# Optimization experiments

Measured on AMD Instinct MI355X. Metric: run time of the kernel, lower is better.

## Reference

```python
import jax, jax.numpy as jnp
import numpy as np
from jax import lax

NUM_GROUPS = 1024
GROUP_SIZE = 32
INIT_DIST = 1e10  # matches torch's 10000000000.0 init


def setup_inputs() -> dict:
    key = jax.random.key(0)
    k1, k2 = jax.random.split(key)
    x = jax.random.normal(k1, (1, 65536, 3), dtype=jnp.float32)
    features = jax.random.normal(k2, (1, 65536, 64), dtype=jnp.float32)
    return {"x": x, "features": features}


def _fps(xyz, npoint):
    # xyz: [B, N, 3] -> centers: [1, npoint, 3] (original code assumes B==1)
    B, N, _ = xyz.shape
    init_dist = jnp.full((B, N), INIT_DIST, dtype=xyz.dtype)
    init_far = jnp.zeros((B,), dtype=jnp.int32)  # deterministic start (torch uses randint)

    def step(carry, _):
        distance, farthest = carry
        centroid = jnp.take_along_axis(xyz, farthest[:, None, None], axis=1)  # [B,1,3]
        dist = jnp.sum((xyz - centroid) ** 2, axis=-1)  # [B,N]
        distance = jnp.minimum(distance, dist)
        new_far = jnp.argmax(distance, axis=-1).astype(jnp.int32)
        return (distance, new_far), farthest

    _, centroids = lax.scan(step, (init_dist, init_far), None, length=npoint)
    centroids = centroids.T  # [B, npoint]
    # original: fps_data = xyz[0, fps_idx].unsqueeze(0)  (B==1 assumption)
    return xyz[0, centroids[0]][None]  # [1, npoint, 3]


def _square_distance(src, dst):
    # src: [B,G,3], dst: [B,N,3] -> [B,G,N]
    d = -2.0 * jnp.einsum("bgc,bnc->bgn", src, dst)
    d += jnp.sum(src ** 2, -1)[:, :, None]
    d += jnp.sum(dst ** 2, -1)[:, None, :]
    return d


def reference(x, features):
    centers = _fps(x, NUM_GROUPS)                 # [1,G,3]
    distances = _square_distance(centers, x)      # [1,G,N]
    _, nb_idx = lax.top_k(-distances, GROUP_SIZE)  # smallest-k -> [1,G,M]
    F = features.shape[-1]
    flat_feat = features.reshape(-1, F)
    neighbors = flat_feat[nb_idx.reshape(-1)].reshape(1, -1, GROUP_SIZE, F)
    nearest_center_idx = jnp.argmin(distances, axis=1)  # [1,N]
    return neighbors, nearest_center_idx
```

## Files before the change

### kernel.cpp

```cpp
#include <hip/hip_runtime.h>
#include <stdint.h>

#define N_PTS   65536
#define N_GRP   1024
#define K_NB    32
#define F_DIM   64

#define FPS1_THR 1024
#define NCHUNK   1024
#define CPTS     64
#define NBINS    4096

#define F2_BLOCKS 16
#define F2_THR    512
#define F2_TT     (F2_BLOCKS*F2_THR)
#define F2_P      (N_PTS / F2_TT)

__device__ __forceinline__ unsigned long long packMinKey(float v, unsigned int idx) {
  unsigned int b = __float_as_uint(v);
  b = (b & 0x80000000u) ? ~b : (b | 0x80000000u);
  return ((unsigned long long)b << 32) | idx;
}
__device__ __forceinline__ float unpackMinVal(unsigned long long k) {
  unsigned int b = (unsigned int)(k >> 32);
  b = (b & 0x80000000u) ? (b & 0x7FFFFFFFu) : ~b;
  return __uint_as_float(b);
}
__device__ __forceinline__ unsigned spread4(unsigned b) {
  return (b & 1u) | ((b & 2u) << 2) | ((b & 4u) << 4) | ((b & 8u) << 6);
}
__device__ __forceinline__ unsigned morton_bid(float a, float b, float c) {
  const float S = 16.0f / 11.0f;
  int bx = (int)((a + 5.5f) * S);
  int by = (int)((b + 5.5f) * S);
  int bz = (int)((c + 5.5f) * S);
  bx = min(max(bx, 0), 15); by = min(max(by, 0), 15); bz = min(max(bz, 0), 15);
  return spread4((unsigned)bx) | (spread4((unsigned)by) << 1) | (spread4((unsigned)bz) << 2);
}

__global__ void __launch_bounds__(FPS1_THR)
fps_kernel(const float* __restrict__ x, float4* __restrict__ xs4,
           float* __restrict__ dd, float* __restrict__ centers)
{
  __shared__ __align__(16) char smem[40960];
  unsigned* sA = (unsigned*)smem;
  unsigned* sB = (unsigned*)(smem + 16384);
  unsigned long long* ckeys = (unsigned long long*)smem;
  unsigned* act = (unsigned*)(smem + 8192);
  float* bxl = (float*)(smem + 12288);
  float* bxh = bxl + 1024;
  float* byl = bxl + 2048;
  float* byh = bxl + 3072;
  float* bzl = bxl + 4096;
  float* bzh = bxl + 5120;
  __shared__ unsigned long long red[16];
  __shared__ int s_nact;

  const int tid = threadIdx.x, lane = tid & 63, wid = tid >> 6;

#pragma unroll
  for (int j = 0; j < NBINS/FPS1_THR; ++j) sA[tid + j*FPS1_THR] = 0u;
  __syncthreads();
  for (int i = tid; i < N_PTS; i += FPS1_THR) {
    float a = x[i*3+0], b = x[i*3+1], c = x[i*3+2];
    atomicAdd(&sA[morton_bid(a,b,c)], 1u);
  }
  __syncthreads();

  {
    unsigned* src = sA; unsigned* dst = sB;
    for (int off = 1; off < NBINS; off <<= 1) {
#pragma unroll
      for (int j = 0; j < NBINS/FPS1_THR; ++j) {
        int i = tid + j*FPS1_THR;
        unsigned v = src[i];
        if (i >= off) v += src[i-off];
        dst[i] = v;
      }
      __syncthreads();
      unsigned* t_ = src; src = dst; dst = t_;
    }
#pragma unroll
    for (int j = 0; j < NBINS/FPS1_THR; ++j) {
      int i = tid + j*FPS1_THR;
      sB[i] = (i == 0) ? 0u : sA[i-1];
    }
    __syncthreads();
  }

  for (int i = tid; i < N_PTS; i += FPS1_THR) {
    float a = x[i*3+0], b = x[i*3+1], c = x[i*3+2];
    unsigned pos = atomicAdd(&sB[morton_bid(a,b,c)], 1u);
    xs4[pos] = make_float4(a, b, c, __uint_as_float((unsigned)i));
    dd[pos]  = 1e10f;
  }
  __syncthreads();

  for (int cc = 0; cc < 64; ++cc) {
    const int c = wid*64 + cc;
    float4 f = xs4[c*CPTS + lane];
    float xl = f.x, xh = f.x, yl = f.y, yh = f.y, zl = f.z, zh = f.z;
#pragma unroll
    for (int off = 32; off; off >>= 1) {
      xl = fminf(xl, __shfl_xor(xl, off)); xh = fmaxf(xh, __shfl_xor(xh, off));
      yl = fminf(yl, __shfl_xor(yl, off)); yh = fmaxf(yh, __shfl_xor(yh, off));
      zl = fminf(zl, __shfl_xor(zl, off)); zh = fmaxf(zh, __shfl_xor(zh, off));
    }
    if (lane == 0) { bxl[c]=xl; bxh[c]=xh; byl[c]=yl; byh[c]=yh; bzl[c]=zl; bzh[c]=zh; }
  }
  __syncthreads();
  const float rxl = bxl[tid], rxh = bxh[tid];
  const float ryl = byl[tid], ryh = byh[tid];
  const float rzl = bzl[tid], rzh = bzh[tid];
  __syncthreads();

  if (tid == 0) s_nact = 0;
  __syncthreads();

  float cx = x[0], cy = x[1], cz = x[2];
  if (tid == 0) { centers[0] = cx; centers[1] = cy; centers[2] = cz; }
  float cdmax = 1e10f;

  for (int r = 1; r < N_GRP; ++r) {
    float dxl = fmaxf(fmaxf(rxl - cx, cx - rxh), 0.0f);
    float dyl = fmaxf(fmaxf(ryl - cy, cy - ryh), 0.0f);
    float dzl = fmaxf(fmaxf(rzl - cz, cz - rzh), 0.0f);
    float b2 = fmaf(dzl, dzl, fmaf(dyl, dyl, dxl*dxl));
    const bool active = b2 < cdmax * 1.0001f;
    const unsigned long long bal = __ballot(active);
    int base = 0;
    if (lane == 0) { int cnt = __popcll(bal); if (cnt) base = atomicAdd(&s_nact, cnt); }
    base = __shfl(base, 0);
    if (active) { int rank = __popcll(bal & ((1ull << lane) - 1ull)); act[base + rank] = (unsigned)tid; }
    __syncthreads();

    const int n = s_nact;
    const int sub = lane >> 4, li = lane & 15;
    for (int bj = wid*4; bj < n; bj += 64) {
      const int jdx = bj + sub;
      const int c = (jdx < n) ? (int)act[jdx] : -1;
      unsigned long long key = 0ull;
      if (c >= 0) {
        const int cb = c*CPTS;
#pragma unroll
        for (int t = 0; t < 4; ++t) {
          const int sidx = cb + li + 16*t;
          float4 f = xs4[sidx];
          float dk = dd[sidx];
          float e0 = f.x - cx, e1 = f.y - cy, e2 = f.z - cz;
          float dist = fmaf(e2,e2, fmaf(e1,e1, e0*e0));
          float dn = fminf(dk, dist);
          dd[sidx] = dn;
          unsigned long long kk = ((unsigned long long)__float_as_uint(dn) << 32)
                                | (unsigned long long)(0xFFFFFFFFu - __float_as_uint(f.w));
          if (kk > key) key = kk;
        }
      }
#pragma unroll
      for (int off = 1; off < 16; off <<= 1) {
        unsigned long long o = __shfl_xor(key, off);
        if (o > key) key = o;
      }
      if (c >= 0 && li == 0) ckeys[c] = key;
    }
    __syncthreads();

    unsigned long long kown = ckeys[tid];
    cdmax = __uint_as_float((unsigned)(kown >> 32));
    unsigned long long k = kown;
#pragma unroll
    for (int off = 32; off; off >>= 1) {
      unsigned long long o = __shfl_xor(k, off);
      if (o > k) k = o;
    }
    if (lane == 0) red[wid] = k;
    if (tid == 0) s_nact = 0;
    __syncthreads();
    unsigned long long k2 = red[lane & 15];
#pragma unroll
    for (int off = 1; off < 16; off <<= 1) {
      unsigned long long o = __shfl_xor(k2, off);
      if (o > k2) k2 = o;
    }
    const unsigned orig = 0xFFFFFFFFu - (unsigned)(k2 & 0xFFFFFFFFull);
    cx = x[orig*3+0]; cy = x[orig*3+1]; cz = x[orig*3+2];
    if (tid == 0) { centers[r*3+0]=cx; centers[r*3+1]=cy; centers[r*3+2]=cz; }
  }
}

__global__ void __launch_bounds__(F2_THR)
fps_safe_kernel(const float* __restrict__ x, unsigned long long* __restrict__ slots,
                unsigned int* __restrict__ cnts, float* __restrict__ centers)
{
  __shared__ unsigned long long red[F2_THR/64];
  const int t = blockIdx.x * F2_THR + threadIdx.x;
  float px[F2_P], py[F2_P], pz[F2_P], d[F2_P];
#pragma unroll
  for (int k = 0; k < F2_P; ++k) {
    int p = t + k * F2_TT;
    px[k] = x[p*3+0]; py[k] = x[p*3+1]; pz[k] = x[p*3+2];
    d[k] = 1e10f;
  }
  float cx = x[0], cy = x[1], cz = x[2];
  if (blockIdx.x == 0 && threadIdx.x == 0) {
    centers[0] = cx; centers[1] = cy; centers[2] = cz;
  }
  for (int r = 1; r < N_GRP; ++r) {
    unsigned long long best = 0ull;
#pragma unroll
    for (int k = 0; k < F2_P; ++k) {
      float e0 = px[k]-cx, e1 = py[k]-cy, e2 = pz[k]-cz;
      float dist = fmaf(e2,e2, fmaf(e1,e1, e0*e0));
      float dn = fminf(d[k], dist);
      d[k] = dn;
      unsigned long long pk = ((unsigned long long)__float_as_uint(dn) << 32)
                            | (0xFFFFFFFFu - (unsigned)(t + k*F2_TT));
      if (pk > best) best = pk;
    }
#pragma unroll
    for (int off = 32; off; off >>= 1) {
      unsigned long long o = __shfl_down(best, off);
      if (o > best) best = o;
    }
    const int wid = threadIdx.x >> 6;
    if ((threadIdx.x & 63) == 0) red[wid] = best;
    __syncthreads();
    if (threadIdx.x == 0) {
#pragma unroll
      for (int w = 1; w < F2_THR/64; ++w) if (red[w] > best) best = red[w];
      atomicMax(&slots[r], best);
      __hip_atomic_fetch_add(&cnts[r], 1u, __ATOMIC_RELEASE, __HIP_MEMORY_SCOPE_AGENT);
      while (__hip_atomic_load(&cnts[r], __ATOMIC_ACQUIRE, __HIP_MEMORY_SCOPE_AGENT) < F2_BLOCKS)
        __builtin_amdgcn_s_sleep(1);
      red[0] = __hip_atomic_load(&slots[r], __ATOMIC_RELAXED, __HIP_MEMORY_SCOPE_AGENT);
    }
    __syncthreads();
    const unsigned long long win = red[0];
    const int widx = (int)(0xFFFFFFFFu - (unsigned int)(win & 0xFFFFFFFFull));
    cx = x[widx*3+0]; cy = x[widx*3+1]; cz = x[widx*3+2];
    if (blockIdx.x == 0 && threadIdx.x == 0) {
      centers[r*3+0] = cx; centers[r*3+1] = cy; centers[r*3+2] = cz;
    }
    __syncthreads();
  }
}

#define TKT 256
#define CAP 3072

__global__ void __launch_bounds__(TKT)
topk_kernel(const float* __restrict__ x, const float* __restrict__ feat,
            const float* __restrict__ centers, float* __restrict__ out)
{
  __shared__ float cv[CAP];
  __shared__ int   ci[CAP];
  __shared__ int   s_cnt;
  __shared__ float s_thr;
  __shared__ float selv[K_NB];
  __shared__ int   seli[K_NB];

  const int g = blockIdx.x, tid = threadIdx.x;
  const float cx = centers[g*3+0], cy = centers[g*3+1], cz = centers[g*3+2];
  const float c2 = fmaf(cz,cz, fmaf(cy,cy, cx*cx));
  if (tid == 0) { s_cnt = 0; s_thr = __builtin_inff(); }
  __syncthreads();

  const int CH = N_PTS / (TKT*8);
  for (int chunk = 0; chunk < CH; ++chunk) {
    const float lthr = s_thr;
#pragma unroll
    for (int k = 0; k < 8; ++k) {
      int p = (chunk*8 + k)*TKT + tid;
      float q0 = x[p*3+0], q1 = x[p*3+1], q2 = x[p*3+2];
      float dot  = fmaf(cz,q2, fmaf(cy,q1, cx*q0));
      float pp   = fmaf(q2,q2, fmaf(q1,q1, q0*q0));
      float dist = fmaf(-2.0f, dot, c2) + pp;
      if (dist <= lthr) {
        int pos = atomicAdd(&s_cnt, 1);
        cv[pos] = dist; ci[pos] = p;
      }
    }
    __syncthreads();
    const int n = s_cnt;
    const bool last = (chunk == CH-1);
    if (n > (CAP - TKT*8) || last) {
      if (tid < 64) {
        for (int it = 0; it < K_NB; ++it) {
          unsigned long long lk = ~0ull;
          for (int j = tid; j < n; j += 64) {
            unsigned long long kk = packMinKey(cv[j], (unsigned)ci[j]);
            if (kk < lk) lk = kk;
          }
#pragma unroll
          for (int off = 32; off; off >>= 1) {
            unsigned long long o = __shfl_xor(lk, off);
            if (o < lk) lk = o;
          }
          const int mi = (int)(unsigned int)(lk & 0xFFFFFFFFull);
          for (int j = tid; j < n; j += 64)
            if (ci[j] == mi) cv[j] = __builtin_inff();
          if (tid == 0) { selv[it] = unpackMinVal(lk); seli[it] = mi; }
        }
      }
      __syncthreads();
      if (!last) {
        if (tid < K_NB) { cv[tid] = selv[tid]; ci[tid] = seli[tid]; }
        if (tid == 0)   { s_cnt = K_NB; s_thr = selv[K_NB-1]; }
        __syncthreads();
      }
    }
  }

  const long base = (long)g * (K_NB*F_DIM);
#pragma unroll
  for (int m = 0; m < (K_NB*F_DIM)/TKT; ++m) {
    int lin = m*TKT + tid;
    int j = lin >> 6, c = lin & 63;
    out[base + lin] = feat[(long)seli[j]*F_DIM + c];
  }
}

__global__ void __launch_bounds__(256)
argmin_kernel(const float* __restrict__ x, const float* __restrict__ centers,
              float* __restrict__ outIdx)
{
  __shared__ float scx[N_GRP], scy[N_GRP], scz[N_GRP], sc2[N_GRP];
  for (int i = threadIdx.x; i < N_GRP; i += 256) {
    float a = centers[i*3+0], b = centers[i*3+1], c = centers[i*3+2];
    scx[i]=a; scy[i]=b; scz[i]=c;
    sc2[i] = fmaf(c,c, fmaf(b,b, a*a));
  }
  __syncthreads();
  const int p = blockIdx.x*256 + threadIdx.x;
  const float q0 = x[p*3+0], q1 = x[p*3+1], q2 = x[p*3+2];
  const float pp = fmaf(q2,q2, fmaf(q1,q1, q0*q0));
  float best = __builtin_inff(); int bi = 0;
#pragma unroll 4
  for (int c = 0; c < N_GRP; ++c) {
    float dot  = fmaf(scz[c],q2, fmaf(scy[c],q1, scx[c]*q0));
    float dist = fmaf(-2.0f, dot, sc2[c]) + pp;
    if (dist < best) { best = dist; bi = c; }
  }
  outIdx[p] = (float)bi;
}

extern "C" void kernel_launch(void* const* d_in, const int* in_sizes, int n_in,
                              void* d_out, int out_size, void* d_ws, size_t ws_size,
                              hipStream_t stream)
{
  const float* x    = (const float*)d_in[0];
  const float* feat = (const float*)d_in[1];
  float* out = (float*)d_out;
  char* ws = (char*)d_ws;

  float* ctr = (float*)ws;
  const size_t DD_OFF  = 65536;
  const size_t XS_OFF  = DD_OFF + (size_t)N_PTS*4;
  const size_t NEED    = XS_OFF + (size_t)N_PTS*16;

  if (ws_size >= NEED) {
    float*  dd  = (float*)(ws + DD_OFF);
    float4* xs4 = (float4*)(ws + XS_OFF);
    hipLaunchKernelGGL(fps_kernel, dim3(1), dim3(FPS1_THR), 0, stream, x, xs4, dd, ctr);
  } else {
    unsigned long long* slots = (unsigned long long*)(ws + 16384);
    unsigned int*       cnts  = (unsigned int*)(ws + 24576);
    hipMemsetAsync(ws + 16384, 0, 12288, stream);
    hipLaunchKernelGGL(fps_safe_kernel, dim3(F2_BLOCKS), dim3(F2_THR), 0, stream,
                       x, slots, cnts, ctr);
  }
  hipLaunchKernelGGL(topk_kernel, dim3(N_GRP), dim3(TKT), 0, stream, x, feat, ctr, out);
  hipLaunchKernelGGL(argmin_kernel, dim3(N_PTS/256), dim3(256), 0, stream,
                     x, ctr, out + (size_t)N_GRP*K_NB*F_DIM);
}
```

Before: 2.986 ms.

## Replace shared active-list compaction with per-wave ballot loops and double-max keys

Each FPS iteration no longer builds a shared-memory list of active chunks with atomics. Each wave now processes its own interleaved chunks straight from its ballot mask, which drops one block-wide barrier and the s_nact atomic per iteration. The 64-bit argmax keys are packed as doubles so fmax replaces the compare-and-select on 64-bit integers. The risks are that work can be uneven across waves, since each wave only handles its own chunks, and that the key keeps only 16 bits of the original index, which relies on N being exactly 65536.

```diff
diff --git a/kernel.cpp b/kernel.cpp
--- a/kernel.cpp
+++ b/kernel.cpp
@@ -37,26 +37,32 @@
   bx = min(max(bx, 0), 15); by = min(max(by, 0), 15); bz = min(max(bz, 0), 15);
   return spread4((unsigned)bx) | (spread4((unsigned)by) << 1) | (spread4((unsigned)bz) << 2);
 }
+__device__ __forceinline__ double packKeyD(float d, unsigned orig, int c) {
+  unsigned long long k = ((unsigned long long)__float_as_uint(d) << 32)
+                       | ((unsigned long long)(0xFFFFu - (orig & 0xFFFFu)) << 16)
+                       | (unsigned long long)(unsigned)c;
+  return __longlong_as_double((long long)k);
+}
 
 __global__ void __launch_bounds__(FPS1_THR)
 fps_kernel(const float* __restrict__ x, float4* __restrict__ xs4,
            float* __restrict__ dd, float* __restrict__ centers)
 {
-  __shared__ __align__(16) char smem[40960];
-  unsigned* sA = (unsigned*)smem;
-  unsigned* sB = (unsigned*)(smem + 16384);
-  unsigned long long* ckeys = (unsigned long long*)smem;
-  unsigned* act = (unsigned*)(smem + 8192);
-  float* bxl = (float*)(smem + 12288);
+  __shared__ __align__(16) char smem[65536];
+  double* ckeys = (double*)smem;
+  float* bxl = (float*)(smem + 8192);
   float* bxh = bxl + 1024;
   float* byl = bxl + 2048;
   float* byh = bxl + 3072;
   float* bzl = bxl + 4096;
   float* bzh = bxl + 5120;
-  __shared__ unsigned long long red[16];
-  __shared__ int s_nact;
+  unsigned* sA = (unsigned*)(smem + 32768);
+  unsigned* sB = (unsigned*)(smem + 49152);
+  __shared__ double redd[16];
 
   const int tid = threadIdx.x, lane = tid & 63, wid = tid >> 6;
+  const int sub = lane >> 4, li = lane & 15;
+  const int cown = 16*lane + wid;
 
 #pragma unroll
   for (int j = 0; j < NBINS/FPS1_THR; ++j) sA[tid + j*FPS1_THR] = 0u;
@@ -109,13 +115,9 @@
     if (lane == 0) { bxl[c]=xl; bxh[c]=xh; byl[c]=yl; byh[c]=yh; bzl[c]=zl; bzh[c]=zh; }
   }
   __syncthreads();
-  const float rxl = bxl[tid], rxh = bxh[tid];
-  const float ryl = byl[tid], ryh = byh[tid];
-  const float rzl = bzl[tid], rzh = bzh[tid];
-  __syncthreads();
-
-  if (tid == 0) s_nact = 0;
-  __syncthreads();
+  const float rxl = bxl[cown], rxh = bxh[cown];
+  const float ryl = byl[cown], ryh = byh[cown];
+  const float rzl = bzl[cown], rzh = bzh[cown];
 
   float cx = x[0], cy = x[1], cz = x[2];
   if (tid == 0) { centers[0] = cx; centers[1] = cy; centers[2] = cz; }
@@ -127,19 +129,17 @@
     float dzl = fmaxf(fmaxf(rzl - cz, cz - rzh), 0.0f);
     float b2 = fmaf(dzl, dzl, fmaf(dyl, dyl, dxl*dxl));
     const bool active = b2 < cdmax * 1.0001f;
-    const unsigned long long bal = __ballot(active);
-    int base = 0;
-    if (lane == 0) { int cnt = __popcll(bal); if (cnt) base = atomicAdd(&s_nact, cnt); }
-    base = __shfl(base, 0);
-    if (active) { int rank = __popcll(bal & ((1ull << lane) - 1ull)); act[base + rank] = (unsigned)tid; }
-    __syncthreads();
-
-    const int n = s_nact;
-    const int sub = lane >> 4, li = lane & 15;
-    for (int bj = wid*4; bj < n; bj += 64) {
-      const int jdx = bj + sub;
-      const int c = (jdx < n) ? (int)act[jdx] : -1;
-      unsigned long long key = 0ull;
+    unsigned long long m = __ballot(active);
+
+    while (m) {
+      int b0 = __ffsll(m) - 1; m &= m - 1;
+      int b1 = -1, b2i = -1, b3 = -1;
+      if (m) { b1  = __ffsll(m) - 1; m &= m - 1; }
+      if (m) { b2i = __ffsll(m) - 1; m &= m - 1; }
+      if (m) { b3  = __ffsll(m) - 1; m &= m - 1; }
+      const int bb = (sub == 0) ? b0 : (sub == 1) ? b1 : (sub == 2) ? b2i : b3;
+      const int c = (bb >= 0) ? (16*bb + wid) : -1;
+      double key = 0.0;
       if (c >= 0) {
         const int cb = c*CPTS;
 #pragma unroll
@@ -151,38 +151,28 @@
           float dist = fmaf(e2,e2, fmaf(e1,e1, e0*e0));
           float dn = fminf(dk, dist);
           dd[sidx] = dn;
-          unsigned long long kk = ((unsigned long long)__float_as_uint(dn) << 32)
-                                | (unsigned long long)(0xFFFFFFFFu - __float_as_uint(f.w));
-          if (kk > key) key = kk;
+          key = fmax(key, packKeyD(dn, __float_as_uint(f.w), c));
         }
       }
 #pragma unroll
-      for (int off = 1; off < 16; off <<= 1) {
-        unsigned long long o = __shfl_xor(key, off);
-        if (o > key) key = o;
-      }
+      for (int off = 1; off < 16; off <<= 1)
+        key = fmax(key, __shfl_xor(key, off));
       if (c >= 0 && li == 0) ckeys[c] = key;
     }
     __syncthreads();
 
-    unsigned long long kown = ckeys[tid];
-    cdmax = __uint_as_float((unsigned)(kown >> 32));
-    unsigned long long k = kown;
-#pragma unroll
-    for (int off = 32; off; off >>= 1) {
-      unsigned long long o = __shfl_xor(k, off);
-      if (o > k) k = o;
-    }
-    if (lane == 0) red[wid] = k;
-    if (tid == 0) s_nact = 0;
-    __syncthreads();
-    unsigned long long k2 = red[lane & 15];
-#pragma unroll
-    for (int off = 1; off < 16; off <<= 1) {
-      unsigned long long o = __shfl_xor(k2, off);
-      if (o > k2) k2 = o;
-    }
-    const unsigned orig = 0xFFFFFFFFu - (unsigned)(k2 & 0xFFFFFFFFull);
+    double kown = ckeys[cown];
+    cdmax = __uint_as_float((unsigned)((unsigned long long)__double_as_longlong(kown) >> 32));
+    double k = kown;
+#pragma unroll
+    for (int off = 32; off; off >>= 1) k = fmax(k, __shfl_xor(k, off));
+    if (lane == 0) redd[wid] = k;
+    __syncthreads();
+    double k2 = redd[lane & 15];
+#pragma unroll
+    for (int off = 1; off < 16; off <<= 1) k2 = fmax(k2, __shfl_xor(k2, off));
+    const unsigned long long kb = (unsigned long long)__double_as_longlong(k2);
+    const unsigned orig = 0xFFFFu - (unsigned)((kb >> 16) & 0xFFFFull);
     cx = x[orig*3+0]; cy = x[orig*3+1]; cz = x[orig*3+2];
     if (tid == 0) { centers[r*3+0]=cx; centers[r*3+1]=cy; centers[r*3+2]=cz; }
   }
```

Measured after the change: 3.096 ms. 3.7% more time.
